# Kernel optimization log

Hardware: AMD Instinct MI355X
Metric: run time of the kernel (lower is better)

## Reference

```python
import jax, jax.numpy as jnp
import numpy as np

D_EMB = 1024
N_HEAD = 16
D_K = D_EMB // N_HEAD


def setup_inputs() -> dict:
    key = jax.random.key(0)
    ks = jax.random.split(key, 11)
    B, S = 2, 2048
    s = 1.0 / np.sqrt(D_EMB)
    inp = {
        'Q': jax.random.normal(ks[0], (B, S, D_EMB), jnp.float32),
        'K': jax.random.normal(ks[1], (B, S, D_EMB), jnp.float32),
        'V': jax.random.normal(ks[2], (B, S, D_EMB), jnp.float32),
        'W_Q': jax.random.normal(ks[3], (D_EMB, D_EMB), jnp.float32) * s,
        'b_Q': jax.random.normal(ks[4], (D_EMB,), jnp.float32) * s,
        'W_K': jax.random.normal(ks[5], (D_EMB, D_EMB), jnp.float32) * s,
        'b_K': jax.random.normal(ks[6], (D_EMB,), jnp.float32) * s,
        'W_V': jax.random.normal(ks[7], (D_EMB, D_EMB), jnp.float32) * s,
        'b_V': jax.random.normal(ks[8], (D_EMB,), jnp.float32) * s,
        'W_O': jax.random.normal(ks[9], (D_EMB, D_EMB), jnp.float32) * s,
        'b_O': jax.random.normal(ks[10], (D_EMB,), jnp.float32) * s,
    }
    return inp


def _heads(x):
    # [B, S, D] -> [B, H, S, d_k]
    B, S, _ = x.shape
    return x.reshape(B, S, N_HEAD, D_K).transpose(0, 2, 1, 3)


def reference(Q, K, V, W_Q, b_Q, W_K, b_K, W_V, b_V, W_O, b_O):
    q = _heads(Q @ W_Q.T + b_Q)
    k = _heads(K @ W_K.T + b_K)
    v = _heads(V @ W_V.T + b_V)
    scale = 1.0 / jnp.sqrt(jnp.asarray(D_K, q.dtype))
    scores = jnp.einsum('bhqd,bhkd->bhqk', q, k) * scale  # [B,H,S,S]
    probs = jax.nn.softmax(scores, axis=-1)
    attn = jnp.einsum('bhqk,bhkd->bhqd', probs, v)
    B, H, S, d = attn.shape
    attn = attn.transpose(0, 2, 1, 3).reshape(B, S, H * d)
    return attn @ W_O.T + b_O
```

## Files before the change

### kernel.cpp

```cpp
#include <hip/hip_runtime.h>
#include <cstdint>
#include <cstddef>

#define S_LEN 2048
#define NH    16
#define DKH   64
#define DEMB  1024
#define MTOT  4096

typedef float f32x4 __attribute__((ext_vector_type(4)));
typedef __bf16 bf16x8 __attribute__((ext_vector_type(8)));
typedef unsigned short u16;
typedef unsigned int u32;
typedef u16 u16x8 __attribute__((ext_vector_type(8)));
typedef u16 u16x4 __attribute__((ext_vector_type(4)));
typedef u32 u32x4 __attribute__((ext_vector_type(4)));

static __device__ __forceinline__ u16 f2bf(float f) {
  u32 u = __builtin_bit_cast(u32, f);
  u += 0x7fffu + ((u >> 16) & 1u);
  return (u16)(u >> 16);
}
static __device__ __forceinline__ bf16x8 ldfrag(const u16* p) {
  return __builtin_bit_cast(bf16x8, *(const u16x8*)p);
}
static __device__ __forceinline__ f32x4 mfma16(bf16x8 a, bf16x8 b, f32x4 c) {
  return __builtin_amdgcn_mfma_f32_16x16x32_bf16(a, b, c, 0, 0, 0);
}
static __device__ __forceinline__ void gl2lds16(const void* g, void* l) {
  __builtin_amdgcn_global_load_lds((__attribute__((address_space(1))) void*)g,
                                   (__attribute__((address_space(3))) void*)l,
                                   16, 0, 0);
}
static __device__ __forceinline__ u32 pkbf(float hi, float lo) {
  u32 a = __builtin_bit_cast(u32, hi) + 0x8000u;
  u32 b = __builtin_bit_cast(u32, lo) + 0x8000u;
  return __builtin_amdgcn_perm(a, b, 0x07060302u);
}
static __device__ __forceinline__ bf16x8 cvt8(f32x4 a, f32x4 b) {
  u32x4 r;
  r[0] = pkbf(a[1], a[0]); r[1] = pkbf(a[3], a[2]);
  r[2] = pkbf(b[1], b[0]); r[3] = pkbf(b[3], b[2]);
  return __builtin_bit_cast(bf16x8, r);
}

#define SCL_Q (0.125f * 1.44269504088896340736f)

__global__ __launch_bounds__(256) void cvt_bf16(const float* __restrict__ s,
                                                u16* __restrict__ d, int n) {
  int i = (blockIdx.x * 256 + threadIdx.x) * 4;
  if (i >= n) return;
  f32x4 f = *(const f32x4*)(s + i);
  u16x4 o;
  o[0] = f2bf(f[0]); o[1] = f2bf(f[1]); o[2] = f2bf(f[2]); o[3] = f2bf(f[3]);
  *(u16x4*)(d + i) = o;
}

__global__ __launch_bounds__(256) void qkv_gemm(
    const float* __restrict__ Qm, const float* __restrict__ Km,
    const float* __restrict__ Vm, const u16* __restrict__ W,
    const float* __restrict__ bq, const float* __restrict__ bk,
    const float* __restrict__ bv,
    u16* __restrict__ qh, u16* __restrict__ kh, u16* __restrict__ vt) {
  __shared__ __align__(16) float sAf[128 * 32];
  __shared__ __align__(16) u16   sB[128 * 32];
  const int t = threadIdx.x;
  const int l = t & 63, w = t >> 6;
  const int ll = l & 15, lg = l >> 4;
  const int nb = blockIdx.x;
  const int mb = blockIdx.y;
  const int which = nb >> 3;
  const float* A = (which == 0) ? Qm : ((which == 1) ? Km : Vm);
  const int wr = (w >> 1) * 64, wc = (w & 1) * 64;

  f32x4 acc[4][4] = {};

  for (int kt = 0; kt < 32; ++kt) {
    const int k0 = kt * 32;
    __syncthreads();
#pragma unroll
    for (int i = 0; i < 4; ++i) {
      const int c = i * 256 + t;
      const int row = c >> 3;
      const int gp = (c >> 1) & 3;
      const int half = c & 1;
      const int gl = gp ^ (row & 3);
      gl2lds16(A + (size_t)(mb * 128 + row) * DEMB + k0 + gl * 8 + half * 4,
               &sAf[c * 4]);
    }
#pragma unroll
    for (int i = 0; i < 2; ++i) {
      const int c = i * 256 + t;
      const int row = c >> 2;
      const int gc = (c & 3) ^ (row & 3);
      gl2lds16(W + (size_t)(nb * 128 + row) * DEMB + k0 + gc * 8, &sB[c * 8]);
    }
    __syncthreads();

    bf16x8 af[4], bfr[4];
#pragma unroll
    for (int i2 = 0; i2 < 4; ++i2) {
      const int row = wr + i2 * 16 + ll;
      const float* p = &sAf[row * 32 + (lg ^ (row & 3)) * 8];
      f32x4 f0 = *(const f32x4*)p;
      f32x4 f1 = *(const f32x4*)(p + 4);
      af[i2] = cvt8(f0, f1);
    }
#pragma unroll
    for (int j2 = 0; j2 < 4; ++j2) {
      const int row = wc + j2 * 16 + ll;
      bfr[j2] = ldfrag(&sB[row * 32 + (lg ^ (row & 3)) * 8]);
    }
#pragma unroll
    for (int i2 = 0; i2 < 4; ++i2)
#pragma unroll
      for (int j2 = 0; j2 < 4; ++j2)
        acc[i2][j2] = mfma16(af[i2], bfr[j2], acc[i2][j2]);
  }

  const float* bias = (which == 0) ? bq : ((which == 1) ? bk : bv);
  const int b = (mb * 128) >> 11;

  if (which == 2) {
#pragma unroll
    for (int j2 = 0; j2 < 4; ++j2) {
      const int nl = (nb * 128 + wc + j2 * 16 + ll) & 1023;
      const int h = nl >> 6, dk = nl & 63;
      const float bb = bias[nl];
      u16* base = vt + ((size_t)((b * NH + h) * DKH + dk)) * S_LEN;
#pragma unroll
      for (int i2 = 0; i2 < 4; ++i2) {
        const int s = (mb * 128 + wr + i2 * 16 + lg * 4) & 2047;
        u16x4 pk;
#pragma unroll
        for (int r = 0; r < 4; ++r) pk[r] = f2bf(acc[i2][j2][r] + bb);
        *(u16x4*)&base[s] = pk;
      }
    }
  } else {
    u16* outp = (which == 0) ? qh : kh;
    const float scl = (which == 0) ? SCL_Q : 1.0f;
#pragma unroll
    for (int j2 = 0; j2 < 4; ++j2) {
      const int nl = (nb * 128 + wc + j2 * 16 + ll) & 1023;
      const int h = nl >> 6, dk = nl & 63;
      const float bb = bias[nl];
#pragma unroll
      for (int i2 = 0; i2 < 4; ++i2) {
#pragma unroll
        for (int r = 0; r < 4; ++r) {
          const int s = (mb * 128 + wr + i2 * 16 + lg * 4 + r) & 2047;
          const float val = (acc[i2][j2][r] + bb) * scl;
          outp[((size_t)((b * NH + h) * S_LEN + s)) * DKH + dk] = f2bf(val);
        }
      }
    }
  }
}

__global__ __launch_bounds__(256) void attn_kernel(
    const u16* __restrict__ qh, const u16* __restrict__ kh,
    const u16* __restrict__ vt, u16* __restrict__ ctx) {
  __shared__ __align__(16) u16 sK[128 * 64];
  __shared__ __align__(16) u16 sV[64 * 128];
  __shared__ __align__(16) u16 sP[4][2][16 * 128];
  const int t = threadIdx.x;
  const int l = t & 63, w = t >> 6;
  const int ll = l & 15, lg = l >> 4;
  const int q_blk = blockIdx.x * 128;
  const int bh = blockIdx.y;

  bf16x8 aq[2][2];
#pragma unroll
  for (int qt = 0; qt < 2; ++qt) {
    const u16* qbase = qh + ((size_t)bh * S_LEN + q_blk + w * 32 + qt * 16 + ll) * DKH;
    aq[qt][0] = ldfrag(qbase + lg * 8);
    aq[qt][1] = ldfrag(qbase + 32 + lg * 8);
  }

  f32x4 oT[2][4] = {};
  float l_part[2] = {0.f, 0.f};

  u16* sP0 = &sP[w][0][0];
  u16* sP1 = &sP[w][1][0];

  for (int kt = 0; kt < 16; ++kt) {
    __syncthreads();
#pragma unroll
    for (int i = 0; i < 4; ++i) {
      const int c = i * 256 + t;
      {
        const int row = c >> 3, gc = (c & 7) ^ (row & 7);
        gl2lds16(kh + ((size_t)bh * S_LEN + kt * 128 + row) * DKH + gc * 8,
                 &sK[c * 8]);
      }
      {
        const int row = c >> 4, gc = (c & 15) ^ (row & 15);
        gl2lds16(vt + ((size_t)bh * DKH + row) * S_LEN + kt * 128 + gc * 8,
                 &sV[c * 8]);
      }
    }
    __syncthreads();

#pragma unroll
    for (int kb = 0; kb < 8; ++kb) {
      const int krow = kb * 16 + ll;
      const bf16x8 ak0 = ldfrag(&sK[krow * 64 + (lg ^ (ll & 7)) * 8]);
      const bf16x8 ak1 = ldfrag(&sK[krow * 64 + ((4 + lg) ^ (ll & 7)) * 8]);
      f32x4 s0 = {}, s1 = {};
      s0 = mfma16(ak0, aq[0][0], s0);
      s0 = mfma16(ak1, aq[0][1], s0);
      s1 = mfma16(ak0, aq[1][0], s1);
      s1 = mfma16(ak1, aq[1][1], s1);
      const int poff = ll * 128 + ((kb ^ (ll & 7)) * 4 + lg) * 4;
      u16x4 pk;
      float ps = 0.f;
#pragma unroll
      for (int r = 0; r < 4; ++r) {
        const float p = __builtin_amdgcn_exp2f(s0[r]);
        ps += p; pk[r] = f2bf(p);
      }
      l_part[0] += ps;
      *(u16x4*)&sP0[poff] = pk;
      ps = 0.f;
#pragma unroll
      for (int r = 0; r < 4; ++r) {
        const float p = __builtin_amdgcn_exp2f(s1[r]);
        ps += p; pk[r] = f2bf(p);
      }
      l_part[1] += ps;
      *(u16x4*)&sP1[poff] = pk;
    }

    bf16x8 bp0[4], bp1[4];
#pragma unroll
    for (int f = 0; f < 4; ++f) {
      const int kb = f * 2 + (lg >> 1);
      const int off = ll * 128 + ((kb ^ (ll & 7)) * 4 + 2 * (lg & 1)) * 4;
      bp0[f] = ldfrag(&sP0[off]);
      bp1[f] = ldfrag(&sP1[off]);
    }
#pragma unroll
    for (int nt = 0; nt < 4; ++nt) {
      const int vrow = nt * 16 + ll;
#pragma unroll
      for (int f = 0; f < 4; ++f) {
        const bf16x8 av = ldfrag(&sV[vrow * 128 + ((f * 4 + lg) ^ ll) * 8]);
        oT[0][nt] = mfma16(av, bp0[f], oT[0][nt]);
        oT[1][nt] = mfma16(av, bp1[f], oT[1][nt]);
      }
    }
  }

  const int b = bh >> 4, h = bh & 15;
#pragma unroll
  for (int qt = 0; qt < 2; ++qt) {
    float lv = l_part[qt];
    lv += __shfl_xor(lv, 16, 64);
    lv += __shfl_xor(lv, 32, 64);
    const float inv = 1.0f / lv;
    const int srow = q_blk + w * 32 + qt * 16 + ll;
#pragma unroll
    for (int nt = 0; nt < 4; ++nt) {
      u16x4 o;
#pragma unroll
      for (int r = 0; r < 4; ++r) o[r] = f2bf(oT[qt][nt][r] * inv);
      *(u16x4*)&ctx[((size_t)((b * S_LEN + srow) * NH + h)) * DKH + nt * 16 + lg * 4] = o;
    }
  }
}

__global__ __launch_bounds__(256) void out_gemm(
    const u16* __restrict__ Am, const u16* __restrict__ W,
    const float* __restrict__ bo, float* __restrict__ out) {
  __shared__ __align__(16) u16 sA[64 * 64];
  __shared__ __align__(16) u16 sB[64 * 64];
  const int t = threadIdx.x;
  const int l = t & 63, w = t >> 6;
  const int ll = l & 15, lg = l >> 4;
  const int nb = blockIdx.x;
  const int mb = blockIdx.y;
  const int wr = (w >> 1) * 32, wc = (w & 1) * 32;

  f32x4 acc[2][2] = {};
  for (int kt = 0; kt < 16; ++kt) {
    const int k0 = kt * 64;
    __syncthreads();
#pragma unroll
    for (int i = 0; i < 2; ++i) {
      const int c = i * 256 + t;
      const int row = c >> 3;
      const int gc = (c & 7) ^ (row & 7);
      gl2lds16(Am + (size_t)(mb * 64 + row) * DEMB + k0 + gc * 8, &sA[c * 8]);
      gl2lds16(W + (size_t)(nb * 64 + row) * DEMB + k0 + gc * 8, &sB[c * 8]);
    }
    __syncthreads();
#pragma unroll
    for (int sub = 0; sub < 2; ++sub) {
      bf16x8 af[2], bfr[2];
#pragma unroll
      for (int i2 = 0; i2 < 2; ++i2) {
        const int row = wr + i2 * 16 + ll;
        af[i2] = ldfrag(&sA[row * 64 + ((sub * 4 + lg) ^ (row & 7)) * 8]);
      }
#pragma unroll
      for (int j2 = 0; j2 < 2; ++j2) {
        const int row = wc + j2 * 16 + ll;
        bfr[j2] = ldfrag(&sB[row * 64 + ((sub * 4 + lg) ^ (row & 7)) * 8]);
      }
#pragma unroll
      for (int i2 = 0; i2 < 2; ++i2)
#pragma unroll
        for (int j2 = 0; j2 < 2; ++j2)
          acc[i2][j2] = mfma16(af[i2], bfr[j2], acc[i2][j2]);
    }
  }

#pragma unroll
  for (int j2 = 0; j2 < 2; ++j2) {
    const int ncol = nb * 64 + wc + j2 * 16 + ll;
    const float bb = bo[ncol];
#pragma unroll
    for (int i2 = 0; i2 < 2; ++i2) {
#pragma unroll
      for (int r = 0; r < 4; ++r) {
        const int mrow = mb * 64 + wr + i2 * 16 + lg * 4 + r;
        out[(size_t)mrow * DEMB + ncol] = acc[i2][j2][r] + bb;
      }
    }
  }
}

extern "C" void kernel_launch(void* const* d_in, const int* in_sizes, int n_in,
                              void* d_out, int out_size, void* d_ws,
                              size_t ws_size, hipStream_t stream) {
  (void)in_sizes; (void)n_in; (void)out_size; (void)ws_size;
  const float* Q  = (const float*)d_in[0];
  const float* K  = (const float*)d_in[1];
  const float* V  = (const float*)d_in[2];
  const float* WQ = (const float*)d_in[3];
  const float* bQ = (const float*)d_in[4];
  const float* WK = (const float*)d_in[5];
  const float* bK = (const float*)d_in[6];
  const float* WV = (const float*)d_in[7];
  const float* bV = (const float*)d_in[8];
  const float* WO = (const float*)d_in[9];
  const float* bO = (const float*)d_in[10];
  float* out = (float*)d_out;

  u16* ws   = (u16*)d_ws;
  u16* Wqkv = ws;
  u16* Wo   = Wqkv + 3072 * 1024;
  u16* qh   = Wo + 1024 * 1024;
  u16* kh   = qh + 32 * 2048 * 64;
  u16* vt   = kh + 32 * 2048 * 64;
  u16* ctx  = vt + 32 * 2048 * 64;

  const int WN = DEMB * DEMB;
  cvt_bf16<<<WN / 1024, 256, 0, stream>>>(WQ, Wqkv, WN);
  cvt_bf16<<<WN / 1024, 256, 0, stream>>>(WK, Wqkv + WN, WN);
  cvt_bf16<<<WN / 1024, 256, 0, stream>>>(WV, Wqkv + 2 * WN, WN);
  cvt_bf16<<<WN / 1024, 256, 0, stream>>>(WO, Wo, WN);

  qkv_gemm<<<dim3(24, 32), 256, 0, stream>>>(Q, K, V, Wqkv, bQ, bK, bV,
                                             qh, kh, vt);
  attn_kernel<<<dim3(16, 32), 256, 0, stream>>>(qh, kh, vt, ctx);
  out_gemm<<<dim3(16, 64), 256, 0, stream>>>(ctx, Wo, bO, out);
}
```

Before: 265.8 us.

## Pre-convert Q/K/V activations to bf16 before the QKV projection GEMM

Adds separate conversion kernels that turn the fp32 Q, K, V inputs into bf16 buffers in workspace. The QKV GEMM then loads bf16 A tiles straight into LDS instead of staging fp32 and converting per tile. The LDS swizzle also changes to XOR on (row>>1)&3 to cut bank conflicts for 64-byte rows. The intent is to halve A-tile LDS traffic and drop redundant conversions, since each A tile is reconverted by all 24 column blocks. The cost is three extra kernel launches and an extra write and read of 48 MB of activations.

```diff
diff --git a/kernel.cpp b/kernel.cpp
--- a/kernel.cpp
+++ b/kernel.cpp
@@ -14,7 +14,6 @@
 typedef unsigned int u32;
 typedef u16 u16x8 __attribute__((ext_vector_type(8)));
 typedef u16 u16x4 __attribute__((ext_vector_type(4)));
-typedef u32 u32x4 __attribute__((ext_vector_type(4)));
 
 static __device__ __forceinline__ u16 f2bf(float f) {
   u32 u = __builtin_bit_cast(u32, f);
@@ -31,17 +30,6 @@
   __builtin_amdgcn_global_load_lds((__attribute__((address_space(1))) void*)g,
                                    (__attribute__((address_space(3))) void*)l,
                                    16, 0, 0);
-}
-static __device__ __forceinline__ u32 pkbf(float hi, float lo) {
-  u32 a = __builtin_bit_cast(u32, hi) + 0x8000u;
-  u32 b = __builtin_bit_cast(u32, lo) + 0x8000u;
-  return __builtin_amdgcn_perm(a, b, 0x07060302u);
-}
-static __device__ __forceinline__ bf16x8 cvt8(f32x4 a, f32x4 b) {
-  u32x4 r;
-  r[0] = pkbf(a[1], a[0]); r[1] = pkbf(a[3], a[2]);
-  r[2] = pkbf(b[1], b[0]); r[3] = pkbf(b[3], b[2]);
-  return __builtin_bit_cast(bf16x8, r);
 }
 
 #define SCL_Q (0.125f * 1.44269504088896340736f)
@@ -57,20 +45,20 @@
 }
 
 __global__ __launch_bounds__(256) void qkv_gemm(
-    const float* __restrict__ Qm, const float* __restrict__ Km,
-    const float* __restrict__ Vm, const u16* __restrict__ W,
+    const u16* __restrict__ qin, const u16* __restrict__ kin,
+    const u16* __restrict__ vin, const u16* __restrict__ W,
     const float* __restrict__ bq, const float* __restrict__ bk,
     const float* __restrict__ bv,
     u16* __restrict__ qh, u16* __restrict__ kh, u16* __restrict__ vt) {
-  __shared__ __align__(16) float sAf[128 * 32];
-  __shared__ __align__(16) u16   sB[128 * 32];
+  __shared__ __align__(16) u16 sA[128 * 32];
+  __shared__ __align__(16) u16 sB[128 * 32];
   const int t = threadIdx.x;
   const int l = t & 63, w = t >> 6;
   const int ll = l & 15, lg = l >> 4;
   const int nb = blockIdx.x;
   const int mb = blockIdx.y;
   const int which = nb >> 3;
-  const float* A = (which == 0) ? Qm : ((which == 1) ? Km : Vm);
+  const u16* A = (which == 0) ? qin : ((which == 1) ? kin : vin);
   const int wr = (w >> 1) * 64, wc = (w & 1) * 64;
 
   f32x4 acc[4][4] = {};
@@ -78,21 +66,12 @@
   for (int kt = 0; kt < 32; ++kt) {
     const int k0 = kt * 32;
     __syncthreads();
-#pragma unroll
-    for (int i = 0; i < 4; ++i) {
-      const int c = i * 256 + t;
-      const int row = c >> 3;
-      const int gp = (c >> 1) & 3;
-      const int half = c & 1;
-      const int gl = gp ^ (row & 3);
-      gl2lds16(A + (size_t)(mb * 128 + row) * DEMB + k0 + gl * 8 + half * 4,
-               &sAf[c * 4]);
-    }
 #pragma unroll
     for (int i = 0; i < 2; ++i) {
       const int c = i * 256 + t;
       const int row = c >> 2;
-      const int gc = (c & 3) ^ (row & 3);
+      const int gc = (c & 3) ^ ((row >> 1) & 3);
+      gl2lds16(A + (size_t)(mb * 128 + row) * DEMB + k0 + gc * 8, &sA[c * 8]);
       gl2lds16(W + (size_t)(nb * 128 + row) * DEMB + k0 + gc * 8, &sB[c * 8]);
     }
     __syncthreads();
@@ -101,15 +80,12 @@
 #pragma unroll
     for (int i2 = 0; i2 < 4; ++i2) {
       const int row = wr + i2 * 16 + ll;
-      const float* p = &sAf[row * 32 + (lg ^ (row & 3)) * 8];
-      f32x4 f0 = *(const f32x4*)p;
-      f32x4 f1 = *(const f32x4*)(p + 4);
-      af[i2] = cvt8(f0, f1);
+      af[i2] = ldfrag(&sA[row * 32 + (lg ^ ((row >> 1) & 3)) * 8]);
     }
 #pragma unroll
     for (int j2 = 0; j2 < 4; ++j2) {
       const int row = wc + j2 * 16 + ll;
-      bfr[j2] = ldfrag(&sB[row * 32 + (lg ^ (row & 3)) * 8]);
+      bfr[j2] = ldfrag(&sB[row * 32 + (lg ^ ((row >> 1) & 3)) * 8]);
     }
 #pragma unroll
     for (int i2 = 0; i2 < 4; ++i2)
@@ -351,18 +327,25 @@
   u16* ws   = (u16*)d_ws;
   u16* Wqkv = ws;
   u16* Wo   = Wqkv + 3072 * 1024;
-  u16* qh   = Wo + 1024 * 1024;
+  u16* qin  = Wo + 1024 * 1024;
+  u16* kin  = qin + (size_t)MTOT * DEMB;
+  u16* vin  = kin + (size_t)MTOT * DEMB;
+  u16* qh   = vin + (size_t)MTOT * DEMB;
   u16* kh   = qh + 32 * 2048 * 64;
   u16* vt   = kh + 32 * 2048 * 64;
   u16* ctx  = vt + 32 * 2048 * 64;
 
   const int WN = DEMB * DEMB;
+  const int AN = MTOT * DEMB;
   cvt_bf16<<<WN / 1024, 256, 0, stream>>>(WQ, Wqkv, WN);
   cvt_bf16<<<WN / 1024, 256, 0, stream>>>(WK, Wqkv + WN, WN);
   cvt_bf16<<<WN / 1024, 256, 0, stream>>>(WV, Wqkv + 2 * WN, WN);
   cvt_bf16<<<WN / 1024, 256, 0, stream>>>(WO, Wo, WN);
-
-  qkv_gemm<<<dim3(24, 32), 256, 0, stream>>>(Q, K, V, Wqkv, bQ, bK, bV,
+  cvt_bf16<<<AN / 1024, 256, 0, stream>>>(Q, qin, AN);
+  cvt_bf16<<<AN / 1024, 256, 0, stream>>>(K, kin, AN);
+  cvt_bf16<<<AN / 1024, 256, 0, stream>>>(V, vin, AN);
+
+  qkv_gemm<<<dim3(24, 32), 256, 0, stream>>>(qin, kin, vin, Wqkv, bQ, bK, bV,
                                              qh, kh, vt);
   attn_kernel<<<dim3(16, 32), 256, 0, stream>>>(qh, kh, vt, ctx);
   out_gemm<<<dim3(16, 64), 256, 0, stream>>>(ctx, Wo, bO, out);
```

Measured after the change: 257.1 us. 3.3% less time.
